# Performance work log

Measured on AMD Instinct MI355X. Metric: run time of the kernel, lower is better.

The kernel has to match this reference:

```python
import jax, jax.numpy as jnp
import numpy as np

N, F, U = 32768, 512, 512
GRID_SIZE, SPLINE_ORDER = 3, 3
GRID_RANGE = (-1.0, 1.0)
LN_EPS = 1e-3  # keras LayerNormalization default epsilon


def _make_grid():
    h = (GRID_RANGE[1] - GRID_RANGE[0]) / GRID_SIZE
    start = -SPLINE_ORDER * h + GRID_RANGE[0]
    stop = (GRID_SIZE + SPLINE_ORDER) * h + GRID_RANGE[0]
    num = GRID_SIZE + 2 * SPLINE_ORDER + 1  # 10 knots
    g = np.linspace(start, stop, num, dtype=np.float32)
    g = np.tile(g, (F, 1))[None, :, :]  # [1, F, num]
    return jnp.asarray(g)


def _glorot(key, shape):
    limit = np.sqrt(6.0 / (shape[0] + shape[1])).astype(np.float32)
    return jax.random.uniform(key, shape, jnp.float32, -limit, limit)


def setup_inputs() -> dict:
    key = jax.random.key(0)
    k_x, k_bw, k_sw = jax.random.split(key, 3)
    return {
        "x": jax.random.normal(k_x, (N, F), jnp.float32),
        "ln_gamma": jnp.ones((F,), jnp.float32),
        "ln_beta": jnp.zeros((F,), jnp.float32),
        "base_weight": _glorot(k_bw, (F, U)),
        "base_bias": jnp.zeros((U,), jnp.float32),
        "spline_weight": _glorot(k_sw, (F * (GRID_SIZE + SPLINE_ORDER), U)),
        "grid": _make_grid(),
    }


def _b_splines(x, grid):
    # x: [N, F]; grid: [1, F, G+2K+1]
    xe = x[..., None]  # [N, F, 1]
    bases = ((xe >= grid[..., :-1]) & (xe < grid[..., 1:])).astype(x.dtype)  # [N,F,G+2K]
    for k in range(1, SPLINE_ORDER + 1):
        left = (xe - grid[..., :-(k + 1)]) / (grid[..., k:-1] - grid[..., :-(k + 1)])
        right = (grid[..., k + 1:] - xe) / (grid[..., k + 1:] - grid[..., 1:-k])
        bases = left * bases[..., :-1] + right * bases[..., 1:]
    return bases.reshape(x.shape[0], -1)  # [N, F*(G+K)]


def reference(x, ln_gamma, ln_beta, base_weight, base_bias, spline_weight, grid):
    # LayerNorm over last axis
    mean = jnp.mean(x, axis=-1, keepdims=True)
    var = jnp.var(x, axis=-1, keepdims=True)
    xn = (x - mean) * jax.lax.rsqrt(var + LN_EPS) * ln_gamma + ln_beta
    # base branch: relu -> matmul -> bias
    base_out = jax.nn.relu(xn) @ base_weight + base_bias
    # spline branch: Cox-de Boor basis -> matmul
    spline_out = _b_splines(xn, grid) @ spline_weight
    # dropout rate 0 / inference -> identity
    return base_out + spline_out
```

## Files before the change

kernel.cpp:

```cpp
#include <hip/hip_runtime.h>
#include <hip/hip_bf16.h>


#define N_ROWS 32768
#define F_DIM  512
#define U_DIM  512
#define K_DIM  4096

typedef short short8 __attribute__((ext_vector_type(8)));
typedef unsigned short ushort8v __attribute__((ext_vector_type(8)));
typedef float floatx4 __attribute__((ext_vector_type(4)));

__device__ __forceinline__ float bf2f(unsigned short h) {
    return __uint_as_float(((unsigned int)h) << 16);
}
__device__ __forceinline__ bool probe_bf16(const void* grid) {
    return ((const unsigned int*)grid)[0] != 0xC0400000u;
}
template <bool B16>
__device__ __forceinline__ float ldf(const void* p, int i) {
    return B16 ? bf2f(((const unsigned short*)p)[i]) : ((const float*)p)[i];
}
template <bool B16>
__device__ __forceinline__ void ld8f(const void* p, int i, float* o) {
    if (B16) {
        ushort8v v = *(const ushort8v*)((const unsigned short*)p + i);
#pragma unroll
        for (int k = 0; k < 8; ++k) o[k] = bf2f(v[k]);
    } else {
        float4 a = *(const float4*)((const float*)p + i);
        float4 b = *(const float4*)((const float*)p + i + 4);
        o[0]=a.x; o[1]=a.y; o[2]=a.z; o[3]=a.w; o[4]=b.x; o[5]=b.y; o[6]=b.z; o[7]=b.w;
    }
}
__device__ __forceinline__ unsigned int pk2(float lo, float hi) {
    __hip_bfloat162 h = __float22bfloat162_rn(make_float2(lo, hi));
    return *reinterpret_cast<unsigned int*>(&h);
}
__device__ __forceinline__ void gld_lds16(const unsigned short* g, unsigned short* l) {
    __builtin_amdgcn_global_load_lds((const __attribute__((address_space(1))) void*)g,
                                     (__attribute__((address_space(3))) void*)l, 16, 0, 0);
}

template <bool B16>
__device__ __forceinline__ void build_wt_body(const void* __restrict__ bw,
                                              const void* __restrict__ sw,
                                              unsigned short* __restrict__ wt, int bid) {
    int idx = bid * 256 + threadIdx.x;
    int u = idx & 511;
    int fq = idx >> 9;
#pragma unroll
    for (int i = 0; i < 4; ++i) {
        int f = fq * 4 + i;
        uint4 w;
        w.x = pk2(ldf<B16>(bw, f * U_DIM + u),            ldf<B16>(sw, (f * 6 + 0) * U_DIM + u));
        w.y = pk2(ldf<B16>(sw, (f * 6 + 1) * U_DIM + u),  ldf<B16>(sw, (f * 6 + 2) * U_DIM + u));
        w.z = pk2(ldf<B16>(sw, (f * 6 + 3) * U_DIM + u),  ldf<B16>(sw, (f * 6 + 4) * U_DIM + u));
        w.w = pk2(ldf<B16>(sw, (f * 6 + 5) * U_DIM + u),  0.f);
        *(uint4*)(wt + (size_t)u * K_DIM + f * 8) = w;
    }
}
__global__ __launch_bounds__(256) void prep_k(const void* __restrict__ bw,
                                              const void* __restrict__ sw,
                                              const void* __restrict__ grid,
                                              unsigned short* __restrict__ wt) {
    if (probe_bf16(grid)) build_wt_body<true>(bw, sw, wt, blockIdx.x);
    else                  build_wt_body<false>(bw, sw, wt, blockIdx.x);
}

__device__ __forceinline__ uint4 spline_pack(float xv, float gv, float bv,
                                             float mean, float rstd) {
    float xn = fmaf(xv - mean, rstd * gv, bv);
    float tt = fmaf(xn, 1.5f, 4.5f);
    float bb[6];
#pragma unroll
    for (int j = 0; j < 6; ++j) {
        float d = tt - (float)(j + 2);
        float a = fabsf(d);
        float a2 = d * d;
        float v1 = fmaf(fmaf(0.5f, a, -1.0f), a2, 0.66666669f);
        float c = fmaxf(2.0f - a, 0.0f);
        float v2 = c * c * c * (1.0f / 6.0f);
        bb[j] = (a < 1.0f) ? v1 : v2;
    }
    uint4 o;
    o.x = pk2(fmaxf(xn, 0.f), bb[0]);
    o.y = pk2(bb[1], bb[2]);
    o.z = pk2(bb[3], bb[4]);
    o.w = pk2(bb[5], 0.f);
    return o;
}

template <bool B16>
__device__ __forceinline__ void kan_gemm_body(
    const void* __restrict__ x,
    const unsigned short* __restrict__ wt,
    const void* __restrict__ gam,
    const void* __restrict__ bet,
    const void* __restrict__ bias,
    void* __restrict__ out,
    unsigned short* __restrict__ Alds,
    unsigned short* __restrict__ Blds,
    float2* __restrict__ gb,
    float2* __restrict__ st) {

    const int tid = threadIdx.x;
    const int lane = tid & 63, wv = tid >> 6;
    const int rtile = blockIdx.x;
    const int lr = lane & 15, lq = lane >> 4;
    const int wr = wv >> 2, wc = wv & 3;

    gb[tid] = make_float2(ldf<B16>(gam, tid), ldf<B16>(bet, tid));

    {
        const int row = tid >> 2, sub = tid & 3;
        const int base = (rtile * 128 + row) * F_DIM + sub * 128;
        float s = 0.f, s2 = 0.f;
#pragma unroll
        for (int i = 0; i < 16; ++i) {
            float v[8];
            ld8f<B16>(x, base + i * 8, v);
#pragma unroll
            for (int k = 0; k < 8; ++k) { s += v[k]; s2 += v[k] * v[k]; }
        }
        s += __shfl_xor(s, 1); s2 += __shfl_xor(s2, 1);
        s += __shfl_xor(s, 2); s2 += __shfl_xor(s2, 2);
        if (sub == 0) {
            float mean = s * (1.0f / F_DIM);
            float var  = s2 * (1.0f / F_DIM) - mean * mean;
            st[row] = make_float2(mean, rsqrtf(var + 1e-3f));
        }
    }

    const unsigned short* gsrc[4];
#pragma unroll
    for (int i = 0; i < 4; ++i) {
        int s = wv * 256 + i * 64 + lane;
        int C = ((s >> 6) << 4) | (s & 15);
        int q = (s >> 4) & 3;
        gsrc[i] = wt + (size_t)C * K_DIM + q * 8;
    }
#pragma unroll
    for (int i = 0; i < 4; ++i)
        gld_lds16(gsrc[i], &Blds[wv * 2048 + i * 512]);

    __syncthreads();

    const int ar = tid & 127, w = tid >> 7;
    const float2 ms = st[ar];
    const float mean = ms.x, rstd = ms.y;
    const int xrow = (rtile * 128 + ar) * F_DIM;
    const int aoff = (ar >> 4) * 512 + w * 128 + (ar & 15) * 8;

    {
        float x0 = ldf<B16>(x, xrow + w);
        float x1 = ldf<B16>(x, xrow + 4 + w);
        float2 ga = gb[w], gc = gb[4 + w];
        *(uint4*)&Alds[aoff]        = spline_pack(x0, ga.x, ga.y, mean, rstd);
        *(uint4*)&Alds[4096 + aoff] = spline_pack(x1, gc.x, gc.y, mean, rstd);
    }
    unsigned short xu0, xu1; float xf0, xf1;
    if (B16) {
        xu0 = ((const unsigned short*)x)[xrow + 8 + w];
        xu1 = ((const unsigned short*)x)[xrow + 12 + w];
    } else {
        xf0 = ((const float*)x)[xrow + 8 + w];
        xf1 = ((const float*)x)[xrow + 12 + w];
    }
    __syncthreads();
    float xC[2];
    if (B16) { xC[0] = bf2f(xu0); xC[1] = bf2f(xu1); }
    else     { xC[0] = xf0;       xC[1] = xf1; }

    floatx4 acc[4][8];
#pragma unroll
    for (int mi = 0; mi < 4; ++mi)
#pragma unroll
        for (int ni = 0; ni < 8; ++ni) acc[mi][ni] = (floatx4){0.f, 0.f, 0.f, 0.f};

    for (int g = 0; g < 64; ++g) {
        unsigned short* __restrict__ Ac = Alds + (g & 1) * 8192;
        unsigned short* __restrict__ An = Alds + ((g & 1) ^ 1) * 8192;
        if (g < 62) {
            int fx = (g + 2) * 8 + w;
            if (B16) {
                xu0 = ((const unsigned short*)x)[xrow + fx];
                xu1 = ((const unsigned short*)x)[xrow + fx + 4];
            } else {
                xf0 = ((const float*)x)[xrow + fx];
                xf1 = ((const float*)x)[xrow + fx + 4];
            }
        }
        const bool dogen = (g < 63);
        const int f0n = (g + 1) * 8 + w;
#pragma unroll
        for (int p = 0; p < 2; ++p) {
            const int ks = g * 2 + p;
            unsigned short* __restrict__ Bc = Blds + (ks & 1) * 16384;
            unsigned short* __restrict__ Bn = Blds + ((ks & 1) ^ 1) * 16384;
            if (ks < 127) {
#pragma unroll
                for (int i = 0; i < 4; ++i)
                    gld_lds16(gsrc[i] + (ks + 1) * 32, &Bn[wv * 2048 + i * 512]);
            }
            short8 afr[4], bfr[8];
#pragma unroll
            for (int mi = 0; mi < 4; ++mi)
                afr[mi] = *(const short8*)&Ac[p * 4096 + ((wr * 4 + mi) * 64 + lane) * 8];
#pragma unroll
            for (int ni = 0; ni < 8; ++ni)
                bfr[ni] = *(const short8*)&Bc[((wc * 8 + ni) * 64 + lane) * 8];
            if (dogen) {
                float2 g2 = gb[f0n + 4 * p];
                *(uint4*)&An[p * 4096 + aoff] =
                    spline_pack(xC[p], g2.x, g2.y, mean, rstd);
            }
            __builtin_amdgcn_s_setprio(1);
#pragma unroll
            for (int mi = 0; mi < 4; ++mi)
#pragma unroll
                for (int ni = 0; ni < 8; ++ni)
                    acc[mi][ni] = __builtin_amdgcn_mfma_f32_16x16x32_bf16(
                        afr[mi], bfr[ni], acc[mi][ni], 0, 0, 0);
            __builtin_amdgcn_s_setprio(0);
            __syncthreads();
        }
        if (g < 62) {
            if (B16) { xC[0] = bf2f(xu0); xC[1] = bf2f(xu1); }
            else     { xC[0] = xf0;       xC[1] = xf1; }
        }
    }

    float biasv[8];
#pragma unroll
    for (int ni = 0; ni < 8; ++ni)
        biasv[ni] = ldf<B16>(bias, wc * 128 + ni * 16 + lr);
#pragma unroll
    for (int mi = 0; mi < 4; ++mi)
#pragma unroll
        for (int ni = 0; ni < 8; ++ni)
#pragma unroll
            for (int r = 0; r < 4; ++r) {
                int row = rtile * 128 + wr * 64 + mi * 16 + lq * 4 + r;
                int col = wc * 128 + ni * 16 + lr;
                float val = acc[mi][ni][r] + biasv[ni];
                if (B16) ((unsigned short*)out)[(size_t)row * U_DIM + col] =
                    (unsigned short)(pk2(val, 0.f) & 0xffffu);
                else ((float*)out)[(size_t)row * U_DIM + col] = val;
            }
}
__global__ __launch_bounds__(512, 2) void kan_gemm(
    const void* __restrict__ x, const unsigned short* __restrict__ wt,
    const void* __restrict__ gam, const void* __restrict__ bet,
    const void* __restrict__ bias, const void* __restrict__ grid,
    void* __restrict__ out) {
    __shared__ __align__(16) unsigned short Alds[2 * 8192];
    __shared__ __align__(16) unsigned short Blds[2 * 16384];
    __shared__ float2 gb_lds[512];
    __shared__ float2 st_lds[128];
    if (probe_bf16(grid))
        kan_gemm_body<true>(x, wt, gam, bet, bias, out, Alds, Blds, gb_lds, st_lds);
    else
        kan_gemm_body<false>(x, wt, gam, bet, bias, out, Alds, Blds, gb_lds, st_lds);
}

extern "C" void kernel_launch(void* const* d_in, const int* in_sizes, int n_in,
                              void* d_out, int out_size, void* d_ws, size_t ws_size,
                              hipStream_t stream) {
    const void* x    = d_in[0];
    const void* gam  = d_in[1];
    const void* bet  = d_in[2];
    const void* bw   = d_in[3];
    const void* bb   = d_in[4];
    const void* sw   = d_in[5];
    const void* grid = d_in[6];

    unsigned short* wt = (unsigned short*)d_ws;

    hipLaunchKernelGGL(prep_k, dim3(U_DIM * 128 / 256), dim3(256), 0, stream,
                       bw, sw, grid, wt);
    hipLaunchKernelGGL(kan_gemm, dim3(N_ROWS / 128), dim3(512), 0, stream,
                       x, wt, gam, bet, bb, grid, d_out);
}
```

Measured before the change: 331.7 us.

## Stage x tiles into LDS via async global_load_lds with double buffering

Replaces the per-thread scalar global loads of upcoming x features with asynchronous 16-byte global-to-LDS loads into a double-buffered staging area. Each thread reads its x value for spline generation from LDS instead. The thread-to-row mapping also changes so that each thread's 4-lane quad computes its own row's mean and rstd, which removes the st LDS array and the extra barrier before those values are read. The intent is better-coalesced x loads and fewer loads in flight per thread inside the GEMM loop. The cost is extra LDS usage and a reliance on the existing per-step barriers to order the async copies.

```diff
diff --git a/kernel.cpp b/kernel.cpp
--- a/kernel.cpp
+++ b/kernel.cpp
@@ -37,7 +37,7 @@
     __hip_bfloat162 h = __float22bfloat162_rn(make_float2(lo, hi));
     return *reinterpret_cast<unsigned int*>(&h);
 }
-__device__ __forceinline__ void gld_lds16(const unsigned short* g, unsigned short* l) {
+__device__ __forceinline__ void gld_lds16(const void* g, void* l) {
     __builtin_amdgcn_global_load_lds((const __attribute__((address_space(1))) void*)g,
                                      (__attribute__((address_space(3))) void*)l, 16, 0, 0);
 }
@@ -102,7 +102,7 @@
     unsigned short* __restrict__ Alds,
     unsigned short* __restrict__ Blds,
     float2* __restrict__ gb,
-    float2* __restrict__ st) {
+    float* __restrict__ xstg) {
 
     const int tid = threadIdx.x;
     const int lane = tid & 63, wv = tid >> 6;
@@ -112,9 +112,10 @@
 
     gb[tid] = make_float2(ldf<B16>(gam, tid), ldf<B16>(bet, tid));
 
+    const int ar = tid >> 2, q = tid & 3;
+    float mean, rstd;
     {
-        const int row = tid >> 2, sub = tid & 3;
-        const int base = (rtile * 128 + row) * F_DIM + sub * 128;
+        const int base = (rtile * 128 + ar) * F_DIM + q * 128;
         float s = 0.f, s2 = 0.f;
 #pragma unroll
         for (int i = 0; i < 16; ++i) {
@@ -125,52 +126,50 @@
         }
         s += __shfl_xor(s, 1); s2 += __shfl_xor(s2, 1);
         s += __shfl_xor(s, 2); s2 += __shfl_xor(s2, 2);
-        if (sub == 0) {
-            float mean = s * (1.0f / F_DIM);
-            float var  = s2 * (1.0f / F_DIM) - mean * mean;
-            st[row] = make_float2(mean, rsqrtf(var + 1e-3f));
-        }
-    }
+        mean = s * (1.0f / F_DIM);
+        float var = s2 * (1.0f / F_DIM) - mean * mean;
+        rstd = rsqrtf(var + 1e-3f);
+    }
+    const int aoff = (ar >> 4) * 512 + q * 128 + (ar & 15) * 8;
 
     const unsigned short* gsrc[4];
 #pragma unroll
     for (int i = 0; i < 4; ++i) {
         int s = wv * 256 + i * 64 + lane;
         int C = ((s >> 6) << 4) | (s & 15);
-        int q = (s >> 4) & 3;
-        gsrc[i] = wt + (size_t)C * K_DIM + q * 8;
+        int qq = (s >> 4) & 3;
+        gsrc[i] = wt + (size_t)C * K_DIM + qq * 8;
     }
 #pragma unroll
     for (int i = 0; i < 4; ++i)
         gld_lds16(gsrc[i], &Blds[wv * 2048 + i * 512]);
 
+    if (B16) {
+        if (wv < 2) {
+            int row = wv * 64 + lane;
+            gld_lds16((const unsigned short*)x + (size_t)(rtile * 128 + row) * F_DIM + 8,
+                      (char*)xstg + wv * 1024);
+        }
+    } else {
+        if (wv < 4) {
+            int s = wv * 64 + lane;
+            int row = s >> 1, hf = s & 1;
+            gld_lds16((const float*)x + (size_t)(rtile * 128 + row) * F_DIM + 8 + hf * 4,
+                      (char*)xstg + wv * 1024);
+        }
+    }
+
+    float x0 = ldf<B16>(x, (rtile * 128 + ar) * F_DIM + q);
+    float x1 = ldf<B16>(x, (rtile * 128 + ar) * F_DIM + 4 + q);
+
     __syncthreads();
 
-    const int ar = tid & 127, w = tid >> 7;
-    const float2 ms = st[ar];
-    const float mean = ms.x, rstd = ms.y;
-    const int xrow = (rtile * 128 + ar) * F_DIM;
-    const int aoff = (ar >> 4) * 512 + w * 128 + (ar & 15) * 8;
-
     {
-        float x0 = ldf<B16>(x, xrow + w);
-        float x1 = ldf<B16>(x, xrow + 4 + w);
-        float2 ga = gb[w], gc = gb[4 + w];
+        float2 ga = gb[q], gc = gb[4 + q];
         *(uint4*)&Alds[aoff]        = spline_pack(x0, ga.x, ga.y, mean, rstd);
         *(uint4*)&Alds[4096 + aoff] = spline_pack(x1, gc.x, gc.y, mean, rstd);
     }
-    unsigned short xu0, xu1; float xf0, xf1;
-    if (B16) {
-        xu0 = ((const unsigned short*)x)[xrow + 8 + w];
-        xu1 = ((const unsigned short*)x)[xrow + 12 + w];
-    } else {
-        xf0 = ((const float*)x)[xrow + 8 + w];
-        xf1 = ((const float*)x)[xrow + 12 + w];
-    }
     __syncthreads();
-    float xC[2];
-    if (B16) { xC[0] = bf2f(xu0); xC[1] = bf2f(xu1); }
-    else     { xC[0] = xf0;       xC[1] = xf1; }
 
     floatx4 acc[4][8];
 #pragma unroll
@@ -181,18 +180,31 @@
     for (int g = 0; g < 64; ++g) {
         unsigned short* __restrict__ Ac = Alds + (g & 1) * 8192;
         unsigned short* __restrict__ An = Alds + ((g & 1) ^ 1) * 8192;
+        const float* __restrict__ xcur = xstg + (g & 1) * 1024;
+        const bool dogen = (g < 63);
+        const int fb = (g + 1) * 8;
+
         if (g < 62) {
-            int fx = (g + 2) * 8 + w;
+            const int fx = (g + 2) * 8;
+            float* __restrict__ xn_ = xstg + ((g & 1) ^ 1) * 1024;
             if (B16) {
-                xu0 = ((const unsigned short*)x)[xrow + fx];
-                xu1 = ((const unsigned short*)x)[xrow + fx + 4];
+                if (wv < 2) {
+                    int row = wv * 64 + lane;
+                    gld_lds16((const unsigned short*)x +
+                                  (size_t)(rtile * 128 + row) * F_DIM + fx,
+                              (char*)xn_ + wv * 1024);
+                }
             } else {
-                xf0 = ((const float*)x)[xrow + fx];
-                xf1 = ((const float*)x)[xrow + fx + 4];
-            }
-        }
-        const bool dogen = (g < 63);
-        const int f0n = (g + 1) * 8 + w;
+                if (wv < 4) {
+                    int s = wv * 64 + lane;
+                    int row = s >> 1, hf = s & 1;
+                    gld_lds16((const float*)x +
+                                  (size_t)(rtile * 128 + row) * F_DIM + fx + hf * 4,
+                              (char*)xn_ + wv * 1024);
+                }
+            }
+        }
+
 #pragma unroll
         for (int p = 0; p < 2; ++p) {
             const int ks = g * 2 + p;
@@ -211,9 +223,11 @@
             for (int ni = 0; ni < 8; ++ni)
                 bfr[ni] = *(const short8*)&Bc[((wc * 8 + ni) * 64 + lane) * 8];
             if (dogen) {
-                float2 g2 = gb[f0n + 4 * p];
-                *(uint4*)&An[p * 4096 + aoff] =
-                    spline_pack(xC[p], g2.x, g2.y, mean, rstd);
+                float xv;
+                if (B16) xv = bf2f(((const unsigned short*)xcur)[ar * 8 + 4 * p + q]);
+                else     xv = xcur[ar * 8 + 4 * p + q];
+                float2 g2 = gb[fb + 4 * p + q];
+                *(uint4*)&An[p * 4096 + aoff] = spline_pack(xv, g2.x, g2.y, mean, rstd);
             }
             __builtin_amdgcn_s_setprio(1);
 #pragma unroll
@@ -224,10 +238,6 @@
                         afr[mi], bfr[ni], acc[mi][ni], 0, 0, 0);
             __builtin_amdgcn_s_setprio(0);
             __syncthreads();
-        }
-        if (g < 62) {
-            if (B16) { xC[0] = bf2f(xu0); xC[1] = bf2f(xu1); }
-            else     { xC[0] = xf0;       xC[1] = xf1; }
         }
     }
 
@@ -257,11 +267,11 @@
     __shared__ __align__(16) unsigned short Alds[2 * 8192];
     __shared__ __align__(16) unsigned short Blds[2 * 16384];
     __shared__ float2 gb_lds[512];
-    __shared__ float2 st_lds[128];
+    __shared__ __align__(16) float xstg_lds[2 * 1024];
     if (probe_bf16(grid))
-        kan_gemm_body<true>(x, wt, gam, bet, bias, out, Alds, Blds, gb_lds, st_lds);
+        kan_gemm_body<true>(x, wt, gam, bet, bias, out, Alds, Blds, gb_lds, xstg_lds);
     else
-        kan_gemm_body<false>(x, wt, gam, bet, bias, out, Alds, Blds, gb_lds, st_lds);
+        kan_gemm_body<false>(x, wt, gam, bet, bias, out, Alds, Blds, gb_lds, xstg_lds);
 }
 
 extern "C" void kernel_launch(void* const* d_in, const int* in_sizes, int n_in,
```

Result: slower. 342.3 us (+3.2%).

## Split GEMM into 128x256 tiles with triple-buffered LDS and fine-grained waits

Applied to the files above, without the earlier changes.

The GEMM kernel now uses 256-thread blocks over a 2-D grid, where each block computes a 128x256 output tile instead of 128x512. The K loop moves from double to triple buffering of A and B in LDS, and each k-step waits with explicit vmcnt/lgkmcnt counts plus a raw s_barrier instead of a full __syncthreads. LayerNorm statistics are now kept in registers per thread rather than shared through LDS. The aim is to raise occupancy and overlap global-to-LDS loads with MFMA work. The cost is that each row tile's LayerNorm and spline generation is recomputed twice, and the hand-placed waitcnt logic is fragile.

```diff
diff --git a/kernel.cpp b/kernel.cpp
--- a/kernel.cpp
+++ b/kernel.cpp
@@ -31,6 +31,16 @@
         float4 a = *(const float4*)((const float*)p + i);
         float4 b = *(const float4*)((const float*)p + i + 4);
         o[0]=a.x; o[1]=a.y; o[2]=a.z; o[3]=a.w; o[4]=b.x; o[5]=b.y; o[6]=b.z; o[7]=b.w;
+    }
+}
+template <bool B16>
+__device__ __forceinline__ void ld2f(const void* p, int i, float& a, float& b) {
+    if (B16) {
+        ushort2 v = *(const ushort2*)((const unsigned short*)p + i);
+        a = bf2f(v.x); b = bf2f(v.y);
+    } else {
+        float2 v = *(const float2*)((const float*)p + i);
+        a = v.x; b = v.y;
     }
 }
 __device__ __forceinline__ unsigned int pk2(float lo, float hi) {
@@ -89,6 +99,62 @@
     o.z = pk2(bb[3], bb[4]);
     o.w = pk2(bb[5], 0.f);
     return o;
+}
+
+template <bool B16, int RR, int RW, bool DOSTG, bool DOX, bool DOGEN, int WAITN, bool DOBAR>
+__device__ __forceinline__ void kstep(
+    int KS, float& xva, float& xvb,
+    unsigned short* __restrict__ Alds, unsigned short* __restrict__ Blds,
+    const float2* __restrict__ gb,
+    const unsigned short* const (&gsrc)[4],
+    const void* __restrict__ x, int xrow, int qh, int aoff0, int aoff1,
+    float mean, float rstd, int wr, int wc, int lane, int wv,
+    floatx4 (&acc)[4][8]) {
+
+    const unsigned short* Ar = Alds + RR * 4096;
+    const unsigned short* Br = Blds + RR * 8192;
+    short8 afr[4], bfr[8];
+#pragma unroll
+    for (int mi = 0; mi < 4; ++mi)
+        afr[mi] = *(const short8*)&Ar[((wr * 4 + mi) * 64 + lane) * 8];
+#pragma unroll
+    for (int ni = 0; ni < 8; ++ni)
+        bfr[ni] = *(const short8*)&Br[((wc * 8 + ni) * 64 + lane) * 8];
+
+    if (DOSTG) {
+        unsigned short* Bw = Blds + RW * 8192;
+#pragma unroll
+        for (int i = 0; i < 4; ++i)
+            gld_lds16(gsrc[i] + (KS + 2) * 32, &Bw[(i * 256 + wv * 64) * 8]);
+    }
+    float xn0 = 0.f, xn1 = 0.f;
+    if (DOX)
+        ld2f<B16>(x, xrow + 4 * (KS + 4) + 2 * qh, xn0, xn1);
+    if (DOGEN) {
+        unsigned short* Aw = Alds + RW * 4096;
+        float4 g4 = *(const float4*)&gb[4 * (KS + 2) + 2 * qh];
+        *(uint4*)&Aw[aoff0] = spline_pack(xva, g4.x, g4.y, mean, rstd);
+        *(uint4*)&Aw[aoff1] = spline_pack(xvb, g4.z, g4.w, mean, rstd);
+    }
+    if (DOX) { xva = xn0; xvb = xn1; }
+
+    __builtin_amdgcn_s_setprio(1);
+#pragma unroll
+    for (int mi = 0; mi < 4; ++mi)
+#pragma unroll
+        for (int ni = 0; ni < 8; ++ni)
+            acc[mi][ni] = __builtin_amdgcn_mfma_f32_16x16x32_bf16(
+                afr[mi], bfr[ni], acc[mi][ni], 0, 0, 0);
+    __builtin_amdgcn_s_setprio(0);
+
+    if (DOBAR) {
+        asm volatile("s_waitcnt lgkmcnt(0)" ::: "memory");
+        if (WAITN == 4) asm volatile("s_waitcnt vmcnt(4)" ::: "memory");
+        else            asm volatile("s_waitcnt vmcnt(0)" ::: "memory");
+        __builtin_amdgcn_sched_barrier(0);
+        __builtin_amdgcn_s_barrier();
+        __builtin_amdgcn_sched_barrier(0);
+    }
 }
 
 template <bool B16>
@@ -101,76 +167,78 @@
     void* __restrict__ out,
     unsigned short* __restrict__ Alds,
     unsigned short* __restrict__ Blds,
-    float2* __restrict__ gb,
-    float2* __restrict__ st) {
+    float2* __restrict__ gb) {
 
     const int tid = threadIdx.x;
     const int lane = tid & 63, wv = tid >> 6;
-    const int rtile = blockIdx.x;
+    const int ctile = blockIdx.x;
+    const int rtile = blockIdx.y;
     const int lr = lane & 15, lq = lane >> 4;
-    const int wr = wv >> 2, wc = wv & 3;
-
-    gb[tid] = make_float2(ldf<B16>(gam, tid), ldf<B16>(bet, tid));
-
+    const int wr = wv >> 1, wc = wv & 1;
+
+    gb[tid]       = make_float2(ldf<B16>(gam, tid),       ldf<B16>(bet, tid));
+    gb[tid + 256] = make_float2(ldf<B16>(gam, tid + 256), ldf<B16>(bet, tid + 256));
+
+    const int ar = tid >> 1, qh = tid & 1;
+    const int xrow = (rtile * 128 + ar) * F_DIM;
+    float mean, rstd;
     {
-        const int row = tid >> 2, sub = tid & 3;
-        const int base = (rtile * 128 + row) * F_DIM + sub * 128;
+        const int base = xrow + qh * 256;
         float s = 0.f, s2 = 0.f;
 #pragma unroll
-        for (int i = 0; i < 16; ++i) {
+        for (int i = 0; i < 32; ++i) {
             float v[8];
             ld8f<B16>(x, base + i * 8, v);
 #pragma unroll
             for (int k = 0; k < 8; ++k) { s += v[k]; s2 += v[k] * v[k]; }
         }
         s += __shfl_xor(s, 1); s2 += __shfl_xor(s2, 1);
-        s += __shfl_xor(s, 2); s2 += __shfl_xor(s2, 2);
-        if (sub == 0) {
-            float mean = s * (1.0f / F_DIM);
-            float var  = s2 * (1.0f / F_DIM) - mean * mean;
-            st[row] = make_float2(mean, rsqrtf(var + 1e-3f));
-        }
-    }
+        mean = s * (1.0f / F_DIM);
+        float var = s2 * (1.0f / F_DIM) - mean * mean;
+        rstd = rsqrtf(var + 1e-3f);
+    }
+    const int aoff0 = ((ar >> 4) * 4 + 2 * qh) * 128 + (ar & 15) * 8;
+    const int aoff1 = aoff0 + 128;
 
     const unsigned short* gsrc[4];
 #pragma unroll
     for (int i = 0; i < 4; ++i) {
-        int s = wv * 256 + i * 64 + lane;
+        int s = tid + i * 256;
         int C = ((s >> 6) << 4) | (s & 15);
         int q = (s >> 4) & 3;
-        gsrc[i] = wt + (size_t)C * K_DIM + q * 8;
-    }
+        gsrc[i] = wt + (size_t)(ctile * 256 + C) * K_DIM + q * 8;
+    }
+
+    float gxa0, gxa1, gxb0, gxb1;
+    ld2f<B16>(x, xrow + 2 * qh, gxa0, gxa1);
+    ld2f<B16>(x, xrow + 4 + 2 * qh, gxb0, gxb1);
 #pragma unroll
     for (int i = 0; i < 4; ++i)
-        gld_lds16(gsrc[i], &Blds[wv * 2048 + i * 512]);
-
-    __syncthreads();
-
-    const int ar = tid & 127, w = tid >> 7;
-    const float2 ms = st[ar];
-    const float mean = ms.x, rstd = ms.y;
-    const int xrow = (rtile * 128 + ar) * F_DIM;
-    const int aoff = (ar >> 4) * 512 + w * 128 + (ar & 15) * 8;
+        gld_lds16(gsrc[i], &Blds[(i * 256 + wv * 64) * 8]);
+    float xv0a, xv0b, xv1a, xv1b;
+    ld2f<B16>(x, xrow + 8 + 2 * qh, xv0a, xv0b);
+#pragma unroll
+    for (int i = 0; i < 4; ++i)
+        gld_lds16(gsrc[i] + 32, &Blds[8192 + (i * 256 + wv * 64) * 8]);
+    ld2f<B16>(x, xrow + 12 + 2 * qh, xv1a, xv1b);
+
+    asm volatile("s_waitcnt lgkmcnt(0)" ::: "memory");
+    __builtin_amdgcn_s_barrier();
+    __builtin_amdgcn_sched_barrier(0);
 
     {
-        float x0 = ldf<B16>(x, xrow + w);
-        float x1 = ldf<B16>(x, xrow + 4 + w);
-        float2 ga = gb[w], gc = gb[4 + w];
-        *(uint4*)&Alds[aoff]        = spline_pack(x0, ga.x, ga.y, mean, rstd);
-        *(uint4*)&Alds[4096 + aoff] = spline_pack(x1, gc.x, gc.y, mean, rstd);
-    }
-    unsigned short xu0, xu1; float xf0, xf1;
-    if (B16) {
-        xu0 = ((const unsigned short*)x)[xrow + 8 + w];
-        xu1 = ((const unsigned short*)x)[xrow + 12 + w];
-    } else {
-        xf0 = ((const float*)x)[xrow + 8 + w];
-        xf1 = ((const float*)x)[xrow + 12 + w];
-    }
-    __syncthreads();
-    float xC[2];
-    if (B16) { xC[0] = bf2f(xu0); xC[1] = bf2f(xu1); }
-    else     { xC[0] = xf0;       xC[1] = xf1; }
+        float4 g0 = *(const float4*)&gb[2 * qh];
+        float4 g1 = *(const float4*)&gb[4 + 2 * qh];
+        *(uint4*)&Alds[aoff0]        = spline_pack(gxa0, g0.x, g0.y, mean, rstd);
+        *(uint4*)&Alds[aoff1]        = spline_pack(gxa1, g0.z, g0.w, mean, rstd);
+        *(uint4*)&Alds[4096 + aoff0] = spline_pack(gxb0, g1.x, g1.y, mean, rstd);
+        *(uint4*)&Alds[4096 + aoff1] = spline_pack(gxb1, g1.z, g1.w, mean, rstd);
+    }
+    asm volatile("s_waitcnt lgkmcnt(0)" ::: "memory");
+    asm volatile("s_waitcnt vmcnt(4)" ::: "memory");
+    __builtin_amdgcn_sched_barrier(0);
+    __builtin_amdgcn_s_barrier();
+    __builtin_amdgcn_sched_barrier(0);
 
     floatx4 acc[4][8];
 #pragma unroll
@@ -178,63 +246,30 @@
 #pragma unroll
         for (int ni = 0; ni < 8; ++ni) acc[mi][ni] = (floatx4){0.f, 0.f, 0.f, 0.f};
 
-    for (int g = 0; g < 64; ++g) {
-        unsigned short* __restrict__ Ac = Alds + (g & 1) * 8192;
-        unsigned short* __restrict__ An = Alds + ((g & 1) ^ 1) * 8192;
-        if (g < 62) {
-            int fx = (g + 2) * 8 + w;
-            if (B16) {
-                xu0 = ((const unsigned short*)x)[xrow + fx];
-                xu1 = ((const unsigned short*)x)[xrow + fx + 4];
-            } else {
-                xf0 = ((const float*)x)[xrow + fx];
-                xf1 = ((const float*)x)[xrow + fx + 4];
-            }
-        }
-        const bool dogen = (g < 63);
-        const int f0n = (g + 1) * 8 + w;
-#pragma unroll
-        for (int p = 0; p < 2; ++p) {
-            const int ks = g * 2 + p;
-            unsigned short* __restrict__ Bc = Blds + (ks & 1) * 16384;
-            unsigned short* __restrict__ Bn = Blds + ((ks & 1) ^ 1) * 16384;
-            if (ks < 127) {
-#pragma unroll
-                for (int i = 0; i < 4; ++i)
-                    gld_lds16(gsrc[i] + (ks + 1) * 32, &Bn[wv * 2048 + i * 512]);
-            }
-            short8 afr[4], bfr[8];
-#pragma unroll
-            for (int mi = 0; mi < 4; ++mi)
-                afr[mi] = *(const short8*)&Ac[p * 4096 + ((wr * 4 + mi) * 64 + lane) * 8];
-#pragma unroll
-            for (int ni = 0; ni < 8; ++ni)
-                bfr[ni] = *(const short8*)&Bc[((wc * 8 + ni) * 64 + lane) * 8];
-            if (dogen) {
-                float2 g2 = gb[f0n + 4 * p];
-                *(uint4*)&An[p * 4096 + aoff] =
-                    spline_pack(xC[p], g2.x, g2.y, mean, rstd);
-            }
-            __builtin_amdgcn_s_setprio(1);
-#pragma unroll
-            for (int mi = 0; mi < 4; ++mi)
-#pragma unroll
-                for (int ni = 0; ni < 8; ++ni)
-                    acc[mi][ni] = __builtin_amdgcn_mfma_f32_16x16x32_bf16(
-                        afr[mi], bfr[ni], acc[mi][ni], 0, 0, 0);
-            __builtin_amdgcn_s_setprio(0);
-            __syncthreads();
-        }
-        if (g < 62) {
-            if (B16) { xC[0] = bf2f(xu0); xC[1] = bf2f(xu1); }
-            else     { xC[0] = xf0;       xC[1] = xf1; }
-        }
-    }
+#define KARGS Alds, Blds, gb, gsrc, x, xrow, qh, aoff0, aoff1, mean, rstd, wr, wc, lane, wv, acc
+#pragma unroll 1
+    for (int kb = 0; kb < 120; kb += 6) {
+        kstep<B16, 0, 2, true, true, true, 4, true>(kb + 0, xv0a, xv0b, KARGS);
+        kstep<B16, 1, 0, true, true, true, 4, true>(kb + 1, xv1a, xv1b, KARGS);
+        kstep<B16, 2, 1, true, true, true, 4, true>(kb + 2, xv0a, xv0b, KARGS);
+        kstep<B16, 0, 2, true, true, true, 4, true>(kb + 3, xv1a, xv1b, KARGS);
+        kstep<B16, 1, 0, true, true, true, 4, true>(kb + 4, xv0a, xv0b, KARGS);
+        kstep<B16, 2, 1, true, true, true, 4, true>(kb + 5, xv1a, xv1b, KARGS);
+    }
+    kstep<B16, 0, 2, true,  true,  true,  4, true>(120, xv0a, xv0b, KARGS);
+    kstep<B16, 1, 0, true,  true,  true,  4, true>(121, xv1a, xv1b, KARGS);
+    kstep<B16, 2, 1, true,  true,  true,  4, true>(122, xv0a, xv0b, KARGS);
+    kstep<B16, 0, 2, true,  true,  true,  4, true>(123, xv1a, xv1b, KARGS);
+    kstep<B16, 1, 0, true,  false, true,  4, true>(124, xv0a, xv0b, KARGS);
+    kstep<B16, 2, 1, true,  false, true,  4, true>(125, xv1a, xv1b, KARGS);
+    kstep<B16, 0, 2, false, false, false, 0, true>(126, xv0a, xv0b, KARGS);
+    kstep<B16, 1, 0, false, false, false, 0, false>(127, xv1a, xv1b, KARGS);
+#undef KARGS
 
     float biasv[8];
 #pragma unroll
     for (int ni = 0; ni < 8; ++ni)
-        biasv[ni] = ldf<B16>(bias, wc * 128 + ni * 16 + lr);
+        biasv[ni] = ldf<B16>(bias, ctile * 256 + wc * 128 + ni * 16 + lr);
 #pragma unroll
     for (int mi = 0; mi < 4; ++mi)
 #pragma unroll
@@ -242,26 +277,25 @@
 #pragma unroll
             for (int r = 0; r < 4; ++r) {
                 int row = rtile * 128 + wr * 64 + mi * 16 + lq * 4 + r;
-                int col = wc * 128 + ni * 16 + lr;
+                int col = ctile * 256 + wc * 128 + ni * 16 + lr;
                 float val = acc[mi][ni][r] + biasv[ni];
                 if (B16) ((unsigned short*)out)[(size_t)row * U_DIM + col] =
                     (unsigned short)(pk2(val, 0.f) & 0xffffu);
                 else ((float*)out)[(size_t)row * U_DIM + col] = val;
             }
 }
-__global__ __launch_bounds__(512, 2) void kan_gemm(
+__global__ __launch_bounds__(256, 2) void kan_gemm(
     const void* __restrict__ x, const unsigned short* __restrict__ wt,
     const void* __restrict__ gam, const void* __restrict__ bet,
     const void* __restrict__ bias, const void* __restrict__ grid,
     void* __restrict__ out) {
-    __shared__ __align__(16) unsigned short Alds[2 * 8192];
-    __shared__ __align__(16) unsigned short Blds[2 * 16384];
-    __shared__ float2 gb_lds[512];
-    __shared__ float2 st_lds[128];
+    __shared__ __align__(16) unsigned short Alds[3 * 4096];
+    __shared__ __align__(16) unsigned short Blds[3 * 8192];
+    __shared__ __align__(16) float2 gb_lds[512];
     if (probe_bf16(grid))
-        kan_gemm_body<true>(x, wt, gam, bet, bias, out, Alds, Blds, gb_lds, st_lds);
+        kan_gemm_body<true>(x, wt, gam, bet, bias, out, Alds, Blds, gb_lds);
     else
-        kan_gemm_body<false>(x, wt, gam, bet, bias, out, Alds, Blds, gb_lds, st_lds);
+        kan_gemm_body<false>(x, wt, gam, bet, bias, out, Alds, Blds, gb_lds);
 }
 
 extern "C" void kernel_launch(void* const* d_in, const int* in_sizes, int n_in,
@@ -279,6 +313,6 @@
 
     hipLaunchKernelGGL(prep_k, dim3(U_DIM * 128 / 256), dim3(256), 0, stream,
                        bw, sw, grid, wt);
-    hipLaunchKernelGGL(kan_gemm, dim3(N_ROWS / 128), dim3(512), 0, stream,
+    hipLaunchKernelGGL(kan_gemm, dim3(2, N_ROWS / 128), dim3(256), 0, stream,
                        x, wt, gam, bet, bb, grid, d_out);
 }
```

Result: slower. 399.8 us (+20.5%).
